# Kernel tuning notes

Measured on AMD Instinct MI355X. Metric: run time of the kernel, lower is better.

## Reference

```python
import jax, jax.numpy as jnp
import numpy as np
import math

HEADS = 8


def rope(t):
    # t: [..., seq, dim]; lucidrains-style interleaved rotary embedding
    seq, dim = t.shape[-2], t.shape[-1]
    inv = 1.0 / (10000.0 ** (jnp.arange(0, dim, 2, dtype=jnp.float32) / dim))
    freqs = jnp.arange(seq, dtype=jnp.float32)[:, None] * inv[None, :]  # [seq, dim/2]
    freqs = jnp.repeat(freqs, 2, axis=-1)                               # [seq, dim]
    cos, sin = jnp.cos(freqs), jnp.sin(freqs)
    t2 = t.reshape(t.shape[:-1] + (dim // 2, 2))
    rot = jnp.stack([-t2[..., 1], t2[..., 0]], axis=-1).reshape(t.shape)
    return t * cos + rot * sin


def conv1x3(x, w):
    # x: [b,c,h,w], w: [out_c,in_c,1,3], padding (0,1), no bias
    return jax.lax.conv_general_dilated(
        x, w, window_strides=(1, 1), padding=((0, 0), (1, 1)),
        dimension_numbers=('NCHW', 'OIHW', 'NCHW'))


def mcl_pw(x, w_pw):
    # per-channel linear on feature axis h: w_pw [c, out_f, in_f]
    return jnp.einsum('bchw,cgh->bcgw', x, w_pw)


def setup_inputs() -> dict:
    key = jax.random.key(0)
    ks = jax.random.split(key, 10)
    b, c, f, w = 2, 8, 256, 1024
    s = 0.05
    return {
        'x': jax.random.normal(ks[0], (b, c, f, w), dtype=jnp.float32),
        'q_pw': jax.random.normal(ks[1], (c, f, f), dtype=jnp.float32) * s,
        'q_cw': jax.random.normal(ks[2], (c, c, 1, 3), dtype=jnp.float32) * s,
        'k_pw': jax.random.normal(ks[3], (c, f, f), dtype=jnp.float32) * s,
        'k_cw': jax.random.normal(ks[4], (c, c, 1, 3), dtype=jnp.float32) * s,
        'v_pw': jax.random.normal(ks[5], (c, f, f), dtype=jnp.float32) * s,
        'v_cw': jax.random.normal(ks[6], (c, c, 1, 3), dtype=jnp.float32) * s,
        'out_pw': jax.random.normal(ks[7], (c, f, f), dtype=jnp.float32) * s,
        'out_dw': jax.random.normal(ks[8], (c, c), dtype=jnp.float32) * s,
    }


def reference(x, q_pw, q_cw, k_pw, k_cw, v_pw, v_cw, out_pw, out_dw):
    b, c, h, w = x.shape
    hd = h // HEADS

    def split_heads(y):  # [b,c,h,w] -> [b,c,heads,w,hd]
        return y.transpose(0, 1, 3, 2).reshape(b, c, w, HEADS, hd).transpose(0, 1, 3, 2, 4)

    q = rope(split_heads(conv1x3(mcl_pw(x, q_pw), q_cw)))
    k = rope(split_heads(conv1x3(mcl_pw(x, k_pw), k_cw)))
    v = split_heads(conv1x3(mcl_pw(x, v_pw), v_cw))

    # non-standard scaling by sqrt(h) = sqrt(features)
    qk = jnp.einsum('bcnqd,bcnkd->bcnqk', q, k) / math.sqrt(h)
    a = jnp.einsum('bcnqk,bcnkd->bcnqd', jax.nn.softmax(qk, axis=-1), v)
    a = a.transpose(0, 1, 3, 2, 4).reshape(b, c, w, h).transpose(0, 1, 3, 2)  # [b,c,h,w]

    # out_proj: depthwise channel mix then per-channel positionwise linear
    out = jnp.einsum('bchw,dc->bdhw', a, out_dw)
    out = mcl_pw(out, out_pw)
    return out
```

## Files before the change

### kernel.cpp

```cpp
#include <hip/hip_runtime.h>
#include <hip/hip_bf16.h>

#define B 2
#define C 8
#define F 256
#define W 1024
#define NH 8
#define HD 32

typedef float f32x4 __attribute__((ext_vector_type(4)));
typedef short sh8 __attribute__((ext_vector_type(8)));
typedef short sh4 __attribute__((ext_vector_type(4)));
typedef unsigned short u16;
typedef unsigned int u32;

#define QSCALE 0.09016843880556021f

static __device__ __forceinline__ float fexp2(float x) {
#if __has_builtin(__builtin_amdgcn_exp2f)
  return __builtin_amdgcn_exp2f(x);
#else
  return __expf(x * 0.69314718056f);
#endif
}

static __device__ __forceinline__ u16 f2b(float x) {
  union { __hip_bfloat16 h; u16 u; } v;
  v.h = __float2bfloat16(x);
  return v.u;
}
static __device__ __forceinline__ sh4 pack4(float p0, float p1, float p2, float p3) {
  union { __hip_bfloat162 h2[2]; sh4 s; } u;
  u.h2[0] = __float22bfloat162_rn(make_float2(p0, p1));
  u.h2[1] = __float22bfloat162_rn(make_float2(p2, p3));
  return u.s;
}
static __device__ __forceinline__ float ubits(u32 u) {
  union { u32 u; float f; } v;
  v.u = u;
  return v.f;
}

static __device__ __forceinline__ f32x4 mfma32(sh8 a, sh8 b, f32x4 c) {
  return __builtin_amdgcn_mfma_f32_16x16x32_bf16(a, b, c, 0, 0, 0);
}

static __device__ __forceinline__ f32x4 mfma16(sh4 a, sh4 b, f32x4 c) {
#if __has_builtin(__builtin_amdgcn_mfma_f32_16x16x16bf16_1k)
  return __builtin_amdgcn_mfma_f32_16x16x16bf16_1k(a, b, c, 0, 0, 0);
#else
  f32x4 d;
  asm("v_mfma_f32_16x16x16_bf16 %0, %1, %2, %3" : "=v"(d) : "v"(a), "v"(b), "v"(c));
  return d;
#endif
}

static __device__ __forceinline__ void gload16(const u16* g, u16* l, int ln) {
#if __has_builtin(__builtin_amdgcn_global_load_lds)
  __builtin_amdgcn_global_load_lds((const __attribute__((address_space(1))) void*)g,
                                   (__attribute__((address_space(3))) void*)l, 16, 0, 0);
#else
  *(sh8*)(l + ln * 8) = *(const sh8*)g;
#endif
}

__global__ __launch_bounds__(256) void prep(const float* __restrict__ x, u16* __restrict__ xt,
                                            const float* __restrict__ s0, const float* __restrict__ s1,
                                            const float* __restrict__ s2, const float* __restrict__ s3,
                                            u16* __restrict__ d0, u16* __restrict__ d1,
                                            u16* __restrict__ d2, u16* __restrict__ d3,
                                            float2* __restrict__ TAB) {
  const int bid = blockIdx.x;
  const int t = threadIdx.x;
  if (bid < 4096) {
    const int bc = bid >> 8, rem = bid & 255;
    const int h0 = ((rem >> 5) & 7) * 32, w0 = (rem & 31) * 32;
    __shared__ u16 sm[32][34];
    const int a = t & 31, bql = t >> 5;
    const float* src = x + ((size_t)bc * F + h0) * W + w0;
#pragma unroll
    for (int p = 0; p < 4; ++p) {
      const int hl = bql + p * 8;
      sm[a][hl] = f2b(src[(size_t)hl * W + a]);
    }
    __syncthreads();
    u16* dst = xt + ((size_t)bc * W + w0) * F + h0;
#pragma unroll
    for (int p = 0; p < 4; ++p) {
      const int wl = bql + p * 8;
      dst[(size_t)wl * F + a] = sm[wl][a];
    }
  } else if (bid < 6144) {
    const int i = bid - 4096;
    const int which = i >> 9;
    const float* s = which == 0 ? s0 : which == 1 ? s1 : which == 2 ? s2 : s3;
    u16* d = which == 0 ? d0 : which == 1 ? d1 : which == 2 ? d2 : d3;
    const int idx = (i & 511) * 256 + t;
    const float4 v = reinterpret_cast<const float4*>(s)[idx];
    union { u16 h[4]; uint2 u; } o;
    o.h[0] = f2b(v.x); o.h[1] = f2b(v.y); o.h[2] = f2b(v.z); o.h[3] = f2b(v.w);
    reinterpret_cast<uint2*>(d)[idx] = o.u;
  } else {
    const int idx = (bid - 6144) * 256 + t;
    const int j = idx >> 10, w = idx & 1023;
    const float inv = powf(10000.f, -(float)(2 * j) / 32.f);
    float sn, cs;
    sincosf((float)w * inv, &sn, &cs);
    TAB[idx] = make_float2(cs, sn);
  }
}

template <bool OUTBF>
__global__ __launch_bounds__(256) void gemm_bt(const u16* __restrict__ Aw,
                                               const u16* __restrict__ Bt,
                                               void* __restrict__ Cc) {
  const int bc = blockIdx.z;
  const int proj = blockIdx.y >> 1;
  const int g0 = (blockIdx.y & 1) * 128;
  const int w0 = blockIdx.x * 64;
  const int t = threadIdx.x;
  const int ln = t & 63, wid = t >> 6;
  const int lr = ln & 15, lk = (ln >> 4) * 8;
  const int wr = wid >> 1, wc = wid & 1;

  const u16* Ab = Aw + (size_t)proj * C * F * F + (size_t)(bc & 7) * F * F;
  const u16* Bb = Bt + (size_t)bc * W * F;

  __shared__ u16 sA[2][8 * 512];
  __shared__ u16 sB[2][4 * 512];

  const u16* ga0 = Ab + (size_t)(g0 + (wid * 2 + 0) * 16 + lr) * F + lk;
  const u16* ga1 = Ab + (size_t)(g0 + (wid * 2 + 1) * 16 + lr) * F + lk;
  const u16* gb0 = Bb + (size_t)(w0 + wid * 16 + lr) * F + lk;

  f32x4 acc[4][2] = {};

  gload16(ga0, &sA[0][(wid * 2 + 0) * 512], ln);
  gload16(ga1, &sA[0][(wid * 2 + 1) * 512], ln);
  gload16(gb0, &sB[0][wid * 512], ln);
  __syncthreads();

  for (int s = 0; s < 8; ++s) {
    const int cur = s & 1;
    if (s < 7) {
      const int h1 = (s + 1) * 32;
      gload16(ga0 + h1, &sA[cur ^ 1][(wid * 2 + 0) * 512], ln);
      gload16(ga1 + h1, &sA[cur ^ 1][(wid * 2 + 1) * 512], ln);
      gload16(gb0 + h1, &sB[cur ^ 1][wid * 512], ln);
    }
    sh8 af[4], bfr[2];
#pragma unroll
    for (int mi = 0; mi < 4; ++mi)
      af[mi] = *(const sh8*)&sA[cur][((wr * 4 + mi) * 64 + ln) * 8];
#pragma unroll
    for (int ni = 0; ni < 2; ++ni)
      bfr[ni] = *(const sh8*)&sB[cur][((wc * 2 + ni) * 64 + ln) * 8];
#pragma unroll
    for (int mi = 0; mi < 4; ++mi)
#pragma unroll
      for (int ni = 0; ni < 2; ++ni)
        acc[mi][ni] = mfma32(af[mi], bfr[ni], acc[mi][ni]);
    __syncthreads();
  }

  const int lq = ln >> 4;
  const size_t cbase = ((size_t)proj * B * C + bc) * F * W;
  if (OUTBF) {
    u16* Cb = (u16*)Cc + cbase;
#pragma unroll
    for (int mi = 0; mi < 4; ++mi)
#pragma unroll
      for (int ni = 0; ni < 2; ++ni)
#pragma unroll
        for (int r = 0; r < 4; ++r)
          Cb[(size_t)(g0 + wr * 64 + mi * 16 + lq * 4 + r) * W + w0 + wc * 32 + ni * 16 + lr] =
              f2b(acc[mi][ni][r]);
  } else {
    float* Cb = (float*)Cc + cbase;
#pragma unroll
    for (int mi = 0; mi < 4; ++mi)
#pragma unroll
      for (int ni = 0; ni < 2; ++ni)
#pragma unroll
        for (int r = 0; r < 4; ++r)
          Cb[(size_t)(g0 + wr * 64 + mi * 16 + lq * 4 + r) * W + w0 + wc * 32 + ni * 16 + lr] =
              acc[mi][ni][r];
  }
}

__global__ __launch_bounds__(256) void conv2(const u16* __restrict__ IN,
                                             const float* __restrict__ CWq,
                                             const float* __restrict__ CWk,
                                             const float* __restrict__ CWv,
                                             const float* __restrict__ TAB,
                                             u16* __restrict__ OUT) {
  const int f2 = blockIdx.x;
  const int z = blockIdx.y;
  const int proj = z >> 1, b = z & 1;
  const float* CW = proj == 0 ? CWq : proj == 1 ? CWk : CWv;
  const size_t NB = (size_t)B * C * F * W;
  const u16* INp = IN + (size_t)proj * NB;
  u16* OUTp = OUT + (size_t)proj * NB;
  const int do_rope = (proj < 2);
  const float scale = (proj == 0) ? QSCALE : 1.0f;
  const int f0 = f2 * 2;
  const int t = threadIdx.x;

  __shared__ u16 s[2][C][1040];
  __shared__ float cw[C][C][3];
  if (t < C * C * 3) ((float*)cw)[t] = CW[t];
  if (t < 16) {
    const int fi = t >> 3, c2 = t & 7;
    s[fi][c2][7] = 0;
    s[fi][c2][1032] = 0;
  }
  {
    const int l = t & 127, rsel = t >> 7;
#pragma unroll
    for (int p = 0; p < 8; ++p) {
      const int row = p * 2 + rsel;
      const int fi = row >> 3, c2 = row & 7;
      const u16* src = INp + ((size_t)(b * C + c2) * F + f0 + fi) * W + l * 8;
      *(sh8*)&s[fi][c2][8 + l * 8] = *(const sh8*)src;
    }
  }
  __syncthreads();

  float acc[2][C][4] = {};
#pragma unroll
  for (int c = 0; c < C; ++c) {
    float v[2][6];
#pragma unroll
    for (int fi = 0; fi < 2; ++fi) {
      const u32* r32 = (const u32*)&s[fi][c][0];
      const u32 r0 = r32[2 * t + 3];
      const u32 r1 = r32[2 * t + 4];
      const u32 r2 = r32[2 * t + 5];
      const u32 r3 = r32[2 * t + 6];
      v[fi][0] = ubits(r0 & 0xffff0000u);
      v[fi][1] = ubits(r1 << 16);
      v[fi][2] = ubits(r1 & 0xffff0000u);
      v[fi][3] = ubits(r2 << 16);
      v[fi][4] = ubits(r2 & 0xffff0000u);
      v[fi][5] = ubits(r3 << 16);
    }
#pragma unroll
    for (int d = 0; d < C; ++d) {
      const float c0 = cw[d][c][0], c1 = cw[d][c][1], c2_ = cw[d][c][2];
#pragma unroll
      for (int fi = 0; fi < 2; ++fi)
#pragma unroll
        for (int o = 0; o < 4; ++o)
          acc[fi][d][o] += v[fi][o] * c0 + v[fi][o + 1] * c1 + v[fi][o + 2] * c2_;
    }
  }

  float cs[4] = {1.f, 1.f, 1.f, 1.f}, sn[4] = {0.f, 0.f, 0.f, 0.f};
  if (do_rope) {
    const int j = f2 & 15;
    const float4* tp = (const float4*)(TAB + (size_t)(j * 1024 + 4 * t) * 2);
    const float4 A0 = tp[0], A1 = tp[1];
    cs[0] = A0.x; sn[0] = A0.y; cs[1] = A0.z; sn[1] = A0.w;
    cs[2] = A1.x; sn[2] = A1.y; cs[3] = A1.z; sn[3] = A1.w;
  }

#pragma unroll
  for (int d = 0; d < C; ++d) {
    sh4 pk0, pk1;
    uint4 pkI;
    u32* pkIa = (u32*)&pkI;
#pragma unroll
    for (int o = 0; o < 4; ++o) {
      const float a0 = acc[0][d][o], a1 = acc[1][d][o];
      float o0 = a0, o1 = a1;
      if (do_rope) { o0 = a0 * cs[o] - a1 * sn[o]; o1 = a1 * cs[o] + a0 * sn[o]; }
      const u16 e0 = f2b(o0 * scale), e1 = f2b(o1 * scale);
      pk0[o] = (short)e0;
      pk1[o] = (short)e1;
      pkIa[o] = (u32)e0 | ((u32)e1 << 16);
    }
    if (proj == 1) {
      *(uint4*)((u32*)OUTp + ((size_t)(b * C + d) * (F / 2) + f2) * W + 4 * t) = pkI;
    } else {
      u16* dst = OUTp + ((size_t)(b * C + d) * F + f0) * W + 4 * t;
      *(sh4*)dst = pk0;
      *(sh4*)(dst + W) = pk1;
    }
  }
}

__global__ __launch_bounds__(1024) void attn_bf(const u16* __restrict__ Q,
                                                const u16* __restrict__ KI,
                                                const u16* __restrict__ Vv,
                                                u16* __restrict__ OT) {
  const int bc = blockIdx.z, n = blockIdx.y, q0 = blockIdx.x * 256;
  const int t = threadIdx.x, ln = t & 63, wid = t >> 6;
  const int lc = ln & 15, g4 = (ln >> 4) * 4;
  const int dq = (ln >> 4) * 8;
  const size_t base = ((size_t)bc * F + n * HD) * W;

  __shared__ u16 Kl[2][64 * 40];
  __shared__ u16 Vl[2][32 * 76];

  const int skey = t & 63, dp = (t >> 6) * 2;
  const u32* gK = (const u32*)KI + ((size_t)bc * (F / 2) + n * 16 + (t >> 6)) * W + skey;
  const int sd = t >> 5, kc2 = (t & 31) * 2;
  const u16* gV = Vv + base + (size_t)sd * W + kc2;

  const int qw = q0 + wid * 16 + lc;
  sh8 qf;
#pragma unroll
  for (int j = 0; j < 8; ++j) qf[j] = (short)Q[base + (size_t)(dq + j) * W + qw];

  const sh4 ones = {0x3F80, 0x3F80, 0x3F80, 0x3F80};
  f32x4 o0 = {0.f, 0.f, 0.f, 0.f}, o1 = {0.f, 0.f, 0.f, 0.f};
  f32x4 dn = {0.f, 0.f, 0.f, 0.f};

  {
    *(u32*)&Kl[0][skey * 40 + dp] = gK[0];
    *(u32*)&Vl[0][sd * 76 + kc2] = *(const u32*)gV;
  }
  __syncthreads();

  for (int tile = 0; tile < 16; ++tile) {
    const int cur = tile & 1;
    u32 hvK = 0, hvV = 0;
    if (tile < 15) {
      const int off = (tile + 1) * 64;
      hvK = gK[off];
      hvV = *(const u32*)(gV + off);
    }

    f32x4 sf[4];
    __builtin_amdgcn_s_setprio(1);
#pragma unroll
    for (int kh = 0; kh < 4; ++kh) {
      const sh8 kf = *(const sh8*)&Kl[cur][(kh * 16 + lc) * 40 + dq];
      f32x4 z = {0.f, 0.f, 0.f, 0.f};
      sf[kh] = mfma32(kf, qf, z);
    }
    __builtin_amdgcn_s_setprio(0);

    sh4 pb[4];
#pragma unroll
    for (int kh = 0; kh < 4; ++kh) {
      const float p0 = fexp2(sf[kh][0]);
      const float p1 = fexp2(sf[kh][1]);
      const float p2 = fexp2(sf[kh][2]);
      const float p3 = fexp2(sf[kh][3]);
      pb[kh] = pack4(p0, p1, p2, p3);
    }

    __builtin_amdgcn_s_setprio(1);
#pragma unroll
    for (int kh = 0; kh < 4; ++kh) {
      const sh4 vf0 = *(const sh4*)&Vl[cur][lc * 76 + kh * 16 + g4];
      const sh4 vf1 = *(const sh4*)&Vl[cur][(16 + lc) * 76 + kh * 16 + g4];
      o0 = mfma16(pb[kh], vf0, o0);
      o1 = mfma16(pb[kh], vf1, o1);
      dn = mfma16(pb[kh], ones, dn);
    }
    __builtin_amdgcn_s_setprio(0);

    if (tile < 15) {
      *(u32*)&Kl[cur ^ 1][skey * 40 + dp] = hvK;
      *(u32*)&Vl[cur ^ 1][sd * 76 + kc2] = hvV;
    }
    __syncthreads();
  }

  const size_t obase = (size_t)bc * W * F + n * HD;
#pragma unroll
  for (int r = 0; r < 4; ++r) {
    const float inv = 1.f / dn[r];
    const int qrow = q0 + wid * 16 + g4 + r;
    OT[obase + (size_t)qrow * F + lc] = f2b(o0[r] * inv);
    OT[obase + (size_t)qrow * F + 16 + lc] = f2b(o1[r] * inv);
  }
}

__global__ __launch_bounds__(256) void chanmix2(const u16* __restrict__ A,
                                                const float* __restrict__ DW,
                                                u16* __restrict__ O1) {
  const int b = blockIdx.y;
  const int w = blockIdx.x * 4 + (threadIdx.x >> 6);
  const int f4 = (threadIdx.x & 63) * 4;
  float dwv[C][C];
#pragma unroll
  for (int d = 0; d < C; ++d)
#pragma unroll
    for (int c = 0; c < C; ++c) dwv[d][c] = DW[d * C + c];

  float av[C][4];
#pragma unroll
  for (int c = 0; c < C; ++c) {
    const uint2 raw = *(const uint2*)&A[(((size_t)(b * C + c)) * W + w) * F + f4];
    av[c][0] = ubits(raw.x << 16);
    av[c][1] = ubits(raw.x & 0xffff0000u);
    av[c][2] = ubits(raw.y << 16);
    av[c][3] = ubits(raw.y & 0xffff0000u);
  }
#pragma unroll
  for (int d = 0; d < C; ++d) {
    float s0 = 0.f, s1 = 0.f, s2 = 0.f, s3 = 0.f;
#pragma unroll
    for (int c = 0; c < C; ++c) {
      s0 += av[c][0] * dwv[d][c];
      s1 += av[c][1] * dwv[d][c];
      s2 += av[c][2] * dwv[d][c];
      s3 += av[c][3] * dwv[d][c];
    }
    *(sh4*)&O1[(((size_t)(b * C + d)) * W + w) * F + f4] = pack4(s0, s1, s2, s3);
  }
}

extern "C" void kernel_launch(void* const* d_in, const int* in_sizes, int n_in,
                              void* d_out, int out_size, void* d_ws, size_t ws_size,
                              hipStream_t stream) {
  const float* x      = (const float*)d_in[0];
  const float* q_pw   = (const float*)d_in[1];
  const float* q_cw   = (const float*)d_in[2];
  const float* k_pw   = (const float*)d_in[3];
  const float* k_cw   = (const float*)d_in[4];
  const float* v_pw   = (const float*)d_in[5];
  const float* v_cw   = (const float*)d_in[6];
  const float* out_pw = (const float*)d_in[7];
  const float* out_dw = (const float*)d_in[8];

  const size_t NB = (size_t)B * C * F * W;
  const size_t CFF = (size_t)C * F * F;

  u16* xt   = (u16*)d_ws;
  u16* wqkv = xt + NB;
  u16* wo   = wqkv + 3 * CFF;
  u16* t0b  = wo + CFF;
  u16* qkvb = t0b + 3 * NB;
  float* tab = (float*)(qkvb + 3 * NB);
  u16* obuf = t0b;
  u16* o1t  = xt;

  prep<<<4096 + 2048 + 64, 256, 0, stream>>>(
      x, xt, q_pw, k_pw, v_pw, out_pw, wqkv, wqkv + CFF, wqkv + 2 * CFF, wo, (float2*)tab);

  gemm_bt<true><<<dim3(W / 64, 6, B * C), 256, 0, stream>>>(wqkv, xt, t0b);
  conv2<<<dim3(F / 2, 3 * B), 256, 0, stream>>>(t0b, q_cw, k_cw, v_cw, tab, qkvb);

  attn_bf<<<dim3(W / 256, NH, B * C), 1024, 0, stream>>>(qkvb, qkvb + NB, qkvb + 2 * NB, obuf);

  chanmix2<<<dim3(W / 4, B), 256, 0, stream>>>(obuf, out_dw, o1t);
  gemm_bt<false><<<dim3(W / 64, 2, B * C), 256, 0, stream>>>(wo, o1t, d_out);
}
```

Before: 99.77 us.

## Load full K and V for a head into LDS once, drop per-tile sync

The attention kernel now stages all 1024 keys of K and V for the head into shared memory at kernel start, replacing the double-buffered 64-key tiles that were refilled each iteration. This removes the 16 per-tile __syncthreads barriers and the interleaved global loads from the inner loop. In exchange it uses roughly 148 KB of LDS per block, which limits residency to one block per CU, and the whole load is exposed up front with no overlap against compute.

```diff
diff --git a/kernel.cpp b/kernel.cpp
--- a/kernel.cpp
+++ b/kernel.cpp
@@ -299,13 +299,25 @@
   const int dq = (ln >> 4) * 8;
   const size_t base = ((size_t)bc * F + n * HD) * W;
 
-  __shared__ u16 Kl[2][64 * 40];
-  __shared__ u16 Vl[2][32 * 76];
-
-  const int skey = t & 63, dp = (t >> 6) * 2;
-  const u32* gK = (const u32*)KI + ((size_t)bc * (F / 2) + n * 16 + (t >> 6)) * W + skey;
-  const int sd = t >> 5, kc2 = (t & 31) * 2;
-  const u16* gV = Vv + base + (size_t)sd * W + kc2;
+  __shared__ u16 Kl[1024 * 40];
+  __shared__ u16 Vl[32 * 1036];
+
+  {
+    const u32* gKI = (const u32*)KI + ((size_t)bc * (F / 2) + n * 16) * W;
+    const u32* gVI = (const u32*)(Vv + base);
+#pragma unroll
+    for (int i = 0; i < 16; ++i) {
+      const int idx = t + i * 1024;
+      const int pl = idx >> 10, key = idx & 1023;
+      *(u32*)&Kl[key * 40 + pl * 2] = gKI[(size_t)pl * W + key];
+    }
+#pragma unroll
+    for (int i = 0; i < 16; ++i) {
+      const int idx = t + i * 1024;
+      const int d = idx >> 9, kp = idx & 511;
+      *(u32*)&Vl[d * 1036 + kp * 2] = gVI[(size_t)d * (W / 2) + kp];
+    }
+  }
 
   const int qw = q0 + wid * 16 + lc;
   sh8 qf;
@@ -316,26 +328,16 @@
   f32x4 o0 = {0.f, 0.f, 0.f, 0.f}, o1 = {0.f, 0.f, 0.f, 0.f};
   f32x4 dn = {0.f, 0.f, 0.f, 0.f};
 
-  {
-    *(u32*)&Kl[0][skey * 40 + dp] = gK[0];
-    *(u32*)&Vl[0][sd * 76 + kc2] = *(const u32*)gV;
-  }
   __syncthreads();
 
   for (int tile = 0; tile < 16; ++tile) {
-    const int cur = tile & 1;
-    u32 hvK = 0, hvV = 0;
-    if (tile < 15) {
-      const int off = (tile + 1) * 64;
-      hvK = gK[off];
-      hvV = *(const u32*)(gV + off);
-    }
+    const int k0 = tile * 64;
 
     f32x4 sf[4];
     __builtin_amdgcn_s_setprio(1);
 #pragma unroll
     for (int kh = 0; kh < 4; ++kh) {
-      const sh8 kf = *(const sh8*)&Kl[cur][(kh * 16 + lc) * 40 + dq];
+      const sh8 kf = *(const sh8*)&Kl[(k0 + kh * 16 + lc) * 40 + dq];
       f32x4 z = {0.f, 0.f, 0.f, 0.f};
       sf[kh] = mfma32(kf, qf, z);
     }
@@ -354,19 +356,13 @@
     __builtin_amdgcn_s_setprio(1);
 #pragma unroll
     for (int kh = 0; kh < 4; ++kh) {
-      const sh4 vf0 = *(const sh4*)&Vl[cur][lc * 76 + kh * 16 + g4];
-      const sh4 vf1 = *(const sh4*)&Vl[cur][(16 + lc) * 76 + kh * 16 + g4];
+      const sh4 vf0 = *(const sh4*)&Vl[lc * 1036 + k0 + kh * 16 + g4];
+      const sh4 vf1 = *(const sh4*)&Vl[(16 + lc) * 1036 + k0 + kh * 16 + g4];
       o0 = mfma16(pb[kh], vf0, o0);
       o1 = mfma16(pb[kh], vf1, o1);
       dn = mfma16(pb[kh], ones, dn);
     }
     __builtin_amdgcn_s_setprio(0);
-
-    if (tile < 15) {
-      *(u32*)&Kl[cur ^ 1][skey * 40 + dp] = hvK;
-      *(u32*)&Vl[cur ^ 1][sd * 76 + kc2] = hvV;
-    }
-    __syncthreads();
   }
 
   const size_t obase = (size_t)bc * W * F + n * HD;
```

Result: slower. 109.4 us (+9.7%).
